# Kernel tuning notes

Measured on AMD Instinct MI355X. Metric: run time of the kernel, lower is better.

The kernel has to match this reference:

```python
import jax, jax.numpy as jnp
import numpy as np
import math

N_NODES = 100000
N_EDGES = 600000
HIDDEN = 128
HEADS = 8
HEAD_DIM = HIDDEN // HEADS
TEMPORAL = 32


def _xavier(key, fan_in, fan_out):
    bound = math.sqrt(6.0 / (fan_in + fan_out))
    return jax.random.uniform(key, (fan_in, fan_out), jnp.float32, -bound, bound)


def setup_inputs() -> dict:
    key = jax.random.key(0)
    ks = jax.random.split(key, 16)
    inp = {
        'query': jax.random.normal(ks[0], (N_NODES, HIDDEN), jnp.float32),
        'key': jax.random.normal(ks[1], (N_NODES, HIDDEN), jnp.float32),
        'value': jax.random.normal(ks[2], (N_NODES, HIDDEN), jnp.float32),
        'temporal_encoding': jax.random.normal(ks[3], (N_EDGES, TEMPORAL), jnp.float32),
        'edge_index': jax.random.randint(ks[4], (2, N_EDGES), 0, N_NODES, jnp.int64),
        # projection weights stored as [in, out] so y = x @ W + b
        'Wq': _xavier(ks[5], HIDDEN, HIDDEN), 'bq': jnp.zeros((HIDDEN,), jnp.float32),
        'Wk': _xavier(ks[6], HIDDEN, HIDDEN), 'bk': jnp.zeros((HIDDEN,), jnp.float32),
        'Wv': _xavier(ks[7], HIDDEN, HIDDEN), 'bv': jnp.zeros((HIDDEN,), jnp.float32),
        'Wtq': _xavier(ks[8], TEMPORAL, HIDDEN), 'btq': jnp.zeros((HIDDEN,), jnp.float32),
        'Wtk': _xavier(ks[9], TEMPORAL, HIDDEN), 'btk': jnp.zeros((HIDDEN,), jnp.float32),
        'Wout': _xavier(ks[10], HIDDEN, HIDDEN), 'bout': jnp.zeros((HIDDEN,), jnp.float32),
    }
    return inp


def reference(query, key, value, temporal_encoding, edge_index,
              Wq, bq, Wk, bk, Wv, bv, Wtq, btq, Wtk, btk, Wout, bout):
    n = query.shape[0]
    H, hd = HEADS, HEAD_DIM
    Q = (query @ Wq + bq).reshape(n, H, hd)
    K = (key @ Wk + bk).reshape(n, H, hd)
    V = (value @ Wv + bv).reshape(n, H, hd)
    tq = (temporal_encoding @ Wtq + btq).reshape(-1, H, hd)
    tk = (temporal_encoding @ Wtk + btk).reshape(-1, H, hd)

    src, tgt = edge_index[0], edge_index[1]
    # per-edge, per-head scores [E, H]
    scores = jnp.sum(Q[src] * K[tgt], axis=-1) / math.sqrt(hd)
    scores = scores + jnp.sum(tq * tk, axis=-1)

    # segment softmax over edges grouped by target node (stable, per head)
    seg_max = jax.ops.segment_max(scores, tgt, num_segments=n)  # [N, H]
    e = jnp.exp(scores - seg_max[tgt])
    seg_sum = jax.ops.segment_sum(e, tgt, num_segments=n)       # [N, H]
    attn_weights = e / seg_sum[tgt]                              # [E, H]

    # weighted scatter-add aggregation of source values onto targets
    agg = jax.ops.segment_sum(attn_weights[..., None] * V[src], tgt, num_segments=n)  # [N, H, hd]
    attn_output = agg.reshape(n, HIDDEN) @ Wout + bout
    return attn_output, attn_weights
```

## Files before the change

### kernel.cpp

```cpp
#include <hip/hip_runtime.h>
#include <hip/hip_bf16.h>

#define HID 128
#define MAXD 64

typedef __attribute__((ext_vector_type(8))) short bfrag8;
typedef __attribute__((ext_vector_type(4))) short bf4;
typedef __attribute__((ext_vector_type(4))) float facc4;

__device__ inline short f2bf(float x) {
  unsigned u = __builtin_bit_cast(unsigned, x);
  u += 0x7fffu + ((u >> 16) & 1u);
  return (short)(u >> 16);
}
__device__ inline float bf2f(short s) {
  unsigned u = ((unsigned)(unsigned short)s) << 16;
  return __builtin_bit_cast(float, u);
}

__device__ inline void store_val(float* Y, size_t i, float v) { Y[i] = v; }
__device__ inline void store_val(short* Y, size_t i, float v) { Y[i] = f2bf(v); }

__global__ __launch_bounds__(256) void init_k(
    const float* __restrict__ Wq, const float* __restrict__ Wk,
    const float* __restrict__ Wv, const float* __restrict__ Wout,
    const float* __restrict__ Wtq, const float* __restrict__ Wtk,
    short* __restrict__ out, int* __restrict__ degcur, int n2) {
  int gid = blockIdx.x * 256 + threadIdx.x;
  if (gid < n2) degcur[gid] = 0;
  if (gid >= 9216) return;
  bfrag8 v;
  if (gid < 8192) {
    int which = gid >> 11;
    int chunk = gid & 2047;
    const float* W = (which == 0) ? Wq : (which == 1) ? Wk
                   : (which == 2) ? Wv : Wout;
    int c  = chunk & 15;
    int g  = (chunk >> 4) & 3;
    int kt = (chunk >> 6) & 3;
    int ct = chunk >> 8;
    int col = ct * 16 + c;
    int k0 = kt * 32 + g * 8;
    #pragma unroll
    for (int i = 0; i < 8; ++i) v[i] = f2bf(W[(size_t)(k0 + i) * HID + col]);
  } else {
    int chunk = gid - 8192;
    int c  = chunk & 15;
    int g  = (chunk >> 4) & 3;
    int ct = (chunk >> 6) & 7;
    int qk = chunk >> 9;
    const float* W = qk ? Wtk : Wtq;
    int col = ct * 16 + c;
    int k0 = g * 8;
    #pragma unroll
    for (int i = 0; i < 8; ++i) v[i] = f2bf(W[(size_t)(k0 + i) * HID + col]);
  }
  *(bfrag8*)(out + (size_t)gid * 8) = v;
}

template <typename IT, typename OT, int MODE>
__device__ __forceinline__ void gemm_body(
    short* __restrict__ Ws, const IT* __restrict__ X,
    const short* __restrict__ Wp, const float* __restrict__ b,
    OT* __restrict__ Y, int nrows, int bx) {
  const int t = threadIdx.x;
  #pragma unroll
  for (int it = 0; it < 8; ++it) {
    int chunk = t + it * 256;
    *(bfrag8*)(&Ws[chunk * 8]) = *(const bfrag8*)(Wp + (size_t)chunk * 8);
  }
  __syncthreads();

  const int w  = t >> 6;
  const int l  = t & 63;
  const int lr = l & 15;
  const int g  = l >> 4;
  const int row0 = bx * 64 + w * 16;
  const int arow = min(row0 + lr, nrows - 1);

  facc4 acc[8];
  #pragma unroll
  for (int i = 0; i < 8; ++i) acc[i] = (facc4){0.f, 0.f, 0.f, 0.f};

  #pragma unroll
  for (int kt = 0; kt < 4; ++kt) {
    bfrag8 a;
    if constexpr (sizeof(IT) == 4) {
      const float* xp = (const float*)X + (size_t)arow * HID + kt * 32 + g * 8;
      float xv[8];
      *(facc4*)(xv)     = *(const facc4*)(xp);
      *(facc4*)(xv + 4) = *(const facc4*)(xp + 4);
      #pragma unroll
      for (int i = 0; i < 8; ++i) a[i] = f2bf(xv[i]);
    } else {
      a = *(const bfrag8*)((const short*)X + (size_t)arow * HID + kt * 32 + g * 8);
    }
    #pragma unroll
    for (int ct = 0; ct < 8; ++ct) {
      bfrag8 bf = *(const bfrag8*)(&Ws[(((ct * 4 + kt) * 4 + g) * 16 + lr) * 8]);
      acc[ct] = __builtin_amdgcn_mfma_f32_16x16x32_bf16(a, bf, acc[ct], 0, 0, 0);
    }
  }

  #pragma unroll
  for (int ct = 0; ct < 8; ++ct) {
    int col = ct * 16 + lr;
    float bias = b[col];
    #pragma unroll
    for (int r = 0; r < 4; ++r) {
      int row = row0 + g * 4 + r;
      if (row < nrows) {
        size_t oidx;
        if constexpr (MODE == 0) oidx = (size_t)row * HID + col;
        else oidx = (size_t)row * 256 + ((col >> 2) << 3) + (col & 3) +
                    (MODE == 2 ? 4 : 0);
        store_val(Y, oidx, acc[ct][r] + bias);
      }
    }
  }
}

__device__ __forceinline__ void temporal_body(
    short* __restrict__ Ws, float* __restrict__ bsh, float* __restrict__ tsh,
    const float* __restrict__ T, const short* __restrict__ Wp,
    const float* __restrict__ btq, const float* __restrict__ btk,
    float* __restrict__ ts, int E, int ntiles, int bx, int nblk) {
  const int t = threadIdx.x;
  #pragma unroll
  for (int it = 0; it < 4; ++it) {
    int chunk = t + it * 256;
    *(bfrag8*)(&Ws[chunk * 8]) = *(const bfrag8*)(Wp + (size_t)chunk * 8);
  }
  bsh[t] = (t < 128) ? btq[t] : btk[t - 128];
  __syncthreads();

  const int w = t >> 6;
  const int l = t & 63;
  const int c = l & 15;
  const int g = l >> 4;
  float* mytsh = tsh + w * 128;

  for (int tile = bx; tile < ntiles; tile += nblk) {
    const int e0 = tile * 64 + w * 16;
    const int ar = min(e0 + c, E - 1);
    const float* tp = T + (size_t)ar * 32 + g * 8;
    float xv[8];
    *(facc4*)(xv)     = *(const facc4*)(tp);
    *(facc4*)(xv + 4) = *(const facc4*)(tp + 4);
    bfrag8 tb;
    #pragma unroll
    for (int i = 0; i < 8; ++i) tb[i] = f2bf(xv[i]);

    #pragma unroll 1
    for (int ct = 0; ct < 8; ++ct) {
      facc4 accq = *(const facc4*)(&bsh[ct * 16 + g * 4]);
      bfrag8 wq = *(const bfrag8*)(&Ws[(ct * 64 + g * 16 + c) * 8]);
      accq = __builtin_amdgcn_mfma_f32_16x16x32_bf16(wq, tb, accq, 0, 0, 0);
      facc4 acck = *(const facc4*)(&bsh[128 + ct * 16 + g * 4]);
      bfrag8 wk = *(const bfrag8*)(&Ws[(512 + ct * 64 + g * 16 + c) * 8]);
      acck = __builtin_amdgcn_mfma_f32_16x16x32_bf16(wk, tb, acck, 0, 0, 0);

      float s = accq[0] * acck[0] + accq[1] * acck[1] +
                accq[2] * acck[2] + accq[3] * acck[3];
      s += __shfl_xor(s, 16, 64);
      s += __shfl_xor(s, 32, 64);
      if (g == 0) mytsh[c * 8 + ct] = s;
    }
    int e = e0 + (l >> 2);
    if (e < E) {
      float2 v2 = *(const float2*)(&mytsh[(l >> 2) * 8 + (l & 3) * 2]);
      *(float2*)(ts + (size_t)e0 * 8 + l * 2) = v2;
    }
  }
}

#define TBLK 2048
__global__ __launch_bounds__(256) void mega_k(
    const float* __restrict__ query, const float* __restrict__ key,
    const float* __restrict__ value, const float* __restrict__ temporal,
    const short* __restrict__ Wpre,
    const float* __restrict__ bq, const float* __restrict__ bk,
    const float* __restrict__ bv, const float* __restrict__ btq,
    const float* __restrict__ btk,
    short* __restrict__ QVp, short* __restrict__ Kp,
    float* __restrict__ tscores, const int* __restrict__ tgt,
    int* __restrict__ deg, int N, int E, int gblk, int ntiles) {
  __shared__ __align__(16) char smem[16384 * 2];
  const int bx = blockIdx.x;
  if (bx < gblk) {
    gemm_body<float, short, 1>((short*)smem, query, Wpre + 0 * 16384, bq, QVp, N, bx);
  } else if (bx < 2 * gblk) {
    gemm_body<float, short, 0>((short*)smem, key, Wpre + 1 * 16384, bk, Kp, N, bx - gblk);
  } else if (bx < 3 * gblk) {
    gemm_body<float, short, 2>((short*)smem, value, Wpre + 2 * 16384, bv, QVp, N, bx - 2 * gblk);
  } else if (bx < 3 * gblk + TBLK) {
    temporal_body((short*)smem, (float*)(smem + 16384), (float*)(smem + 16384 + 1024),
                  temporal, Wpre + 4 * 16384, btq, btk, tscores, E, ntiles,
                  bx - 3 * gblk, TBLK);
  } else {
    int gid = (bx - 3 * gblk - TBLK) * 256 + threadIdx.x;
    if (gid < E) atomicAdd(&deg[tgt[gid]], 1);
  }
}

template <typename IT, typename OT, int MODE>
__global__ __launch_bounds__(256) void gemm_mfma_k(
    const IT* __restrict__ X, const short* __restrict__ Wp,
    const float* __restrict__ b, OT* __restrict__ Y, int nrows) {
  __shared__ __align__(16) short Ws[16384];
  gemm_body<IT, OT, MODE>(Ws, X, Wp, b, Y, nrows, blockIdx.x);
}

__global__ __launch_bounds__(256) void block_sum_k(const int* __restrict__ deg,
                                                   int* __restrict__ bsum, int n) {
  __shared__ int sd[256];
  const int base = blockIdx.x * 1024;
  const int t = threadIdx.x;
  int s = 0;
  #pragma unroll
  for (int j = 0; j < 4; ++j) {
    int i = base + t + j * 256;
    if (i < n) s += deg[i];
  }
  sd[t] = s;
  __syncthreads();
  for (int st = 128; st; st >>= 1) {
    if (t < st) sd[t] += sd[t + st];
    __syncthreads();
  }
  if (t == 0) bsum[blockIdx.x] = sd[0];
}

__global__ __launch_bounds__(1024) void scan_partials_k(const int* __restrict__ bsum,
                                                        int* __restrict__ boff, int G) {
  __shared__ int sd[1024];
  const int t = threadIdx.x;
  int v = (t < G) ? bsum[t] : 0;
  sd[t] = v;
  __syncthreads();
  for (int s = 1; s < 1024; s <<= 1) {
    int a = (t >= s) ? sd[t - s] : 0;
    __syncthreads();
    sd[t] += a;
    __syncthreads();
  }
  if (t < G) boff[t] = sd[t] - v;
}

__global__ __launch_bounds__(256) void block_scan_k(const int* __restrict__ deg,
                                                    const int* __restrict__ boff,
                                                    int* __restrict__ off, int n) {
  __shared__ int sd[256];
  const int base = blockIdx.x * 1024;
  const int t = threadIdx.x;
  const int i0 = base + t * 4;
  int v[4];
  int s = 0;
  #pragma unroll
  for (int j = 0; j < 4; ++j) {
    v[j] = (i0 + j < n) ? deg[i0 + j] : 0;
    s += v[j];
  }
  const int own = s;
  sd[t] = s;
  __syncthreads();
  for (int st = 1; st < 256; st <<= 1) {
    int a = (t >= st) ? sd[t - st] : 0;
    __syncthreads();
    sd[t] += a;
    __syncthreads();
  }
  int acc = boff[blockIdx.x] + sd[t] - own;
  #pragma unroll
  for (int j = 0; j < 4; ++j) {
    int idx = i0 + j;
    if (idx < n) {
      off[idx] = acc;
      acc += v[j];
      if (idx == n - 1) off[n] = acc;
    }
  }
}

__global__ __launch_bounds__(256) void scatter_k(const int* __restrict__ src,
                                                 const int* __restrict__ tgt,
                                                 const int* __restrict__ off,
                                                 int* __restrict__ cur,
                                                 int2* __restrict__ elist2, int E) {
  int gid = blockIdx.x * 256 + threadIdx.x;
  if (gid < E) {
    int n = tgt[gid];
    int p = atomicAdd(&cur[n], 1);
    elist2[off[n] + p] = make_int2(gid, src[gid]);
  }
}

__global__ __launch_bounds__(256) void softmax_agg_k(
    const float* __restrict__ tscores, const short* __restrict__ QVp,
    const short* __restrict__ Kp, const int* __restrict__ off,
    const int2* __restrict__ elist2, float* __restrict__ attn_w,
    short* __restrict__ aggb, int N) {
  __shared__ int esh[8][MAXD];
  __shared__ int ssh[8][MAXD];
  __shared__ float sraw[8][MAXD][8];
  const int t = threadIdx.x;
  const int grp = t >> 5;
  const int g = t & 31;
  const int h = g >> 2;
  const int j = g & 3;
  const int n = blockIdx.x * 8 + grp;
  if (n >= N) return;

  const int s0 = off[n];
  const int deg = off[n + 1] - s0;

  float kr[4];
  {
    bf4 k4 = *(const bf4*)(Kp + (size_t)n * HID + g * 4);
    #pragma unroll
    for (int q = 0; q < 4; ++q) kr[q] = bf2f(k4[q]);
  }

  if (deg <= MAXD) {
    for (int i = g; i < deg; i += 32) {
      int2 es = elist2[s0 + i];
      esh[grp][i] = es.x;
      ssh[grp][i] = es.y;
    }

    float lsum = 0.f;
    float a0 = 0.f, a1 = 0.f, a2 = 0.f, a3 = 0.f;
    int i = 0;
    for (; i + 4 <= deg; i += 4) {
      bfrag8 qv0 = *(const bfrag8*)(QVp + (size_t)ssh[grp][i]     * 256 + g * 8);
      bfrag8 qv1 = *(const bfrag8*)(QVp + (size_t)ssh[grp][i + 1] * 256 + g * 8);
      bfrag8 qv2 = *(const bfrag8*)(QVp + (size_t)ssh[grp][i + 2] * 256 + g * 8);
      bfrag8 qv3 = *(const bfrag8*)(QVp + (size_t)ssh[grp][i + 3] * 256 + g * 8);
      float ts0 = tscores[(size_t)esh[grp][i]     * 8 + h];
      float ts1 = tscores[(size_t)esh[grp][i + 1] * 8 + h];
      float ts2 = tscores[(size_t)esh[grp][i + 2] * 8 + h];
      float ts3 = tscores[(size_t)esh[grp][i + 3] * 8 + h];
      float p0 = bf2f(qv0[0]) * kr[0] + bf2f(qv0[1]) * kr[1] +
                 bf2f(qv0[2]) * kr[2] + bf2f(qv0[3]) * kr[3];
      float p1 = bf2f(qv1[0]) * kr[0] + bf2f(qv1[1]) * kr[1] +
                 bf2f(qv1[2]) * kr[2] + bf2f(qv1[3]) * kr[3];
      float p2 = bf2f(qv2[0]) * kr[0] + bf2f(qv2[1]) * kr[1] +
                 bf2f(qv2[2]) * kr[2] + bf2f(qv2[3]) * kr[3];
      float p3 = bf2f(qv3[0]) * kr[0] + bf2f(qv3[1]) * kr[1] +
                 bf2f(qv3[2]) * kr[2] + bf2f(qv3[3]) * kr[3];
      p0 += __shfl_xor(p0, 1, 4); p0 += __shfl_xor(p0, 2, 4);
      p1 += __shfl_xor(p1, 1, 4); p1 += __shfl_xor(p1, 2, 4);
      p2 += __shfl_xor(p2, 1, 4); p2 += __shfl_xor(p2, 2, 4);
      p3 += __shfl_xor(p3, 1, 4); p3 += __shfl_xor(p3, 2, 4);
      float w0 = __expf(ts0 + p0 * 0.25f);
      float w1 = __expf(ts1 + p1 * 0.25f);
      float w2 = __expf(ts2 + p2 * 0.25f);
      float w3 = __expf(ts3 + p3 * 0.25f);
      if (j == 0) {
        sraw[grp][i][h]     = w0;
        sraw[grp][i + 1][h] = w1;
        sraw[grp][i + 2][h] = w2;
        sraw[grp][i + 3][h] = w3;
      }
      lsum += (w0 + w1) + (w2 + w3);
      a0 += w0 * bf2f(qv0[4]) + w1 * bf2f(qv1[4]) +
            w2 * bf2f(qv2[4]) + w3 * bf2f(qv3[4]);
      a1 += w0 * bf2f(qv0[5]) + w1 * bf2f(qv1[5]) +
            w2 * bf2f(qv2[5]) + w3 * bf2f(qv3[5]);
      a2 += w0 * bf2f(qv0[6]) + w1 * bf2f(qv1[6]) +
            w2 * bf2f(qv2[6]) + w3 * bf2f(qv3[6]);
      a3 += w0 * bf2f(qv0[7]) + w1 * bf2f(qv1[7]) +
            w2 * bf2f(qv2[7]) + w3 * bf2f(qv3[7]);
    }
    for (; i < deg; ++i) {
      bfrag8 qv0 = *(const bfrag8*)(QVp + (size_t)ssh[grp][i] * 256 + g * 8);
      float ts0 = tscores[(size_t)esh[grp][i] * 8 + h];
      float p0 = bf2f(qv0[0]) * kr[0] + bf2f(qv0[1]) * kr[1] +
                 bf2f(qv0[2]) * kr[2] + bf2f(qv0[3]) * kr[3];
      p0 += __shfl_xor(p0, 1, 4); p0 += __shfl_xor(p0, 2, 4);
      float w0 = __expf(ts0 + p0 * 0.25f);
      if (j == 0) sraw[grp][i][h] = w0;
      lsum += w0;
      a0 += w0 * bf2f(qv0[4]);
      a1 += w0 * bf2f(qv0[5]);
      a2 += w0 * bf2f(qv0[6]);
      a3 += w0 * bf2f(qv0[7]);
    }
    float invl = (lsum > 0.f) ? 1.0f / lsum : 0.f;

    bf4 st;
    st[0] = f2bf(a0 * invl); st[1] = f2bf(a1 * invl);
    st[2] = f2bf(a2 * invl); st[3] = f2bf(a3 * invl);
    *(bf4*)(aggb + (size_t)n * HID + g * 4) = st;

    if (j == 0) {
      for (int q = 0; q < deg; ++q)
        attn_w[(size_t)esh[grp][q] * 8 + h] = sraw[grp][q][h] * invl;
    }
  } else {
    float m = -3.0e38f;
    for (int q = 0; q < deg; ++q) {
      int2 es = elist2[s0 + q];
      bfrag8 q4 = *(const bfrag8*)(QVp + (size_t)es.y * 256 + g * 8);
      float p = bf2f(q4[0]) * kr[0] + bf2f(q4[1]) * kr[1] +
                bf2f(q4[2]) * kr[2] + bf2f(q4[3]) * kr[3];
      p += __shfl_xor(p, 1, 4); p += __shfl_xor(p, 2, 4);
      m = fmaxf(m, tscores[(size_t)es.x * 8 + h] + p * 0.25f);
    }
    float l = 0.f;
    for (int q = 0; q < deg; ++q) {
      int2 es = elist2[s0 + q];
      bfrag8 q4 = *(const bfrag8*)(QVp + (size_t)es.y * 256 + g * 8);
      float p = bf2f(q4[0]) * kr[0] + bf2f(q4[1]) * kr[1] +
                bf2f(q4[2]) * kr[2] + bf2f(q4[3]) * kr[3];
      p += __shfl_xor(p, 1, 4); p += __shfl_xor(p, 2, 4);
      l += __expf(tscores[(size_t)es.x * 8 + h] + p * 0.25f - m);
    }
    float invl = (l > 0.f) ? 1.0f / l : 0.f;
    float a0 = 0.f, a1 = 0.f, a2 = 0.f, a3 = 0.f;
    for (int q = 0; q < deg; ++q) {
      int2 es = elist2[s0 + q];
      bfrag8 q4 = *(const bfrag8*)(QVp + (size_t)es.y * 256 + g * 8);
      float p = bf2f(q4[0]) * kr[0] + bf2f(q4[1]) * kr[1] +
                bf2f(q4[2]) * kr[2] + bf2f(q4[3]) * kr[3];
      p += __shfl_xor(p, 1, 4); p += __shfl_xor(p, 2, 4);
      float w = __expf(tscores[(size_t)es.x * 8 + h] + p * 0.25f - m) * invl;
      a0 += w * bf2f(q4[4]);
      a1 += w * bf2f(q4[5]);
      a2 += w * bf2f(q4[6]);
      a3 += w * bf2f(q4[7]);
      if (j == 0) attn_w[(size_t)es.x * 8 + h] = w;
    }
    bf4 st;
    st[0] = f2bf(a0); st[1] = f2bf(a1); st[2] = f2bf(a2); st[3] = f2bf(a3);
    *(bf4*)(aggb + (size_t)n * HID + g * 4) = st;
  }
}

extern "C" void kernel_launch(void* const* d_in, const int* in_sizes, int n_in,
                              void* d_out, int out_size, void* d_ws, size_t ws_size,
                              hipStream_t stream) {
  const float* query    = (const float*)d_in[0];
  const float* key      = (const float*)d_in[1];
  const float* value    = (const float*)d_in[2];
  const float* temporal = (const float*)d_in[3];
  const int*   eidx     = (const int*)d_in[4];
  const float* Wq   = (const float*)d_in[5];
  const float* bq   = (const float*)d_in[6];
  const float* Wk   = (const float*)d_in[7];
  const float* bk   = (const float*)d_in[8];
  const float* Wv   = (const float*)d_in[9];
  const float* bv   = (const float*)d_in[10];
  const float* Wtq  = (const float*)d_in[11];
  const float* btq  = (const float*)d_in[12];
  const float* Wtk  = (const float*)d_in[13];
  const float* btk  = (const float*)d_in[14];
  const float* Wout = (const float*)d_in[15];
  const float* bout = (const float*)d_in[16];

  const int N = in_sizes[0] / HID;
  const int E = in_sizes[4] / 2;
  const int* src = eidx;
  const int* tgt = eidx + E;

  char* ws = (char*)d_ws;
  short* QVp = (short*)ws;                     ws += (size_t)N * 256 * 2;
  short* Kp = (short*)ws;                      ws += (size_t)N * HID * 2;
  short* aggb = (short*)ws;                    ws += (size_t)N * HID * 2;
  float* tscores = (float*)ws;                 ws += (size_t)E * 8 * 4;
  int* deg   = (int*)ws;                       ws += (size_t)N * 4;
  int* cur   = (int*)ws;                       ws += (size_t)N * 4;
  int* off   = (int*)ws;                       ws += (size_t)(N + 2) * 4;
  int2* elist2 = (int2*)ws;                    ws += (size_t)E * 8;
  int* bsum  = (int*)ws;                       ws += 1024 * 4;
  int* boff  = (int*)ws;                       ws += 1024 * 4;
  short* Wpre = (short*)ws;

  const int G = (N + 1023) / 1024;
  const int gblk = (N + 63) / 64;
  const int ntiles = (E + 63) / 64;
  const int cblk = (E + 255) / 256;

  dim3 b256(256);
  init_k<<<(2 * N + 255) / 256, b256, 0, stream>>>(Wq, Wk, Wv, Wout, Wtq, Wtk,
                                                   Wpre, deg, 2 * N);
  mega_k<<<3 * gblk + TBLK + cblk, b256, 0, stream>>>(
      query, key, value, temporal, Wpre, bq, bk, bv, btq, btk,
      QVp, Kp, tscores, tgt, deg, N, E, gblk, ntiles);

  block_sum_k<<<G, b256, 0, stream>>>(deg, bsum, N);
  scan_partials_k<<<1, 1024, 0, stream>>>(bsum, boff, G);
  block_scan_k<<<G, b256, 0, stream>>>(deg, boff, off, N);
  scatter_k<<<cblk, b256, 0, stream>>>(src, tgt, off, cur, elist2, E);

  float* attn_w = (float*)d_out + (size_t)N * HID;
  softmax_agg_k<<<(N + 7) / 8, b256, 0, stream>>>(tscores, QVp, Kp, off,
                                                  elist2, attn_w, aggb, N);

  gemm_mfma_k<short, float, 0><<<gblk, b256, 0, stream>>>(aggb, Wpre + 3 * 16384, bout,
                                                          (float*)d_out, N);
}
```

Before: 261.6 us.

## Persistent GEMM blocks, transposed MFMA output with vector stores, split QV layout

The projection GEMMs now loop over several 64-row chunks per block (a quarter as many blocks), so each block loads the packed weights into LDS once and reuses them. The MFMA operands are swapped so each lane holds four consecutive output columns of one row, which allows vectorized bias loads and 4-wide stores. The interleaved Q/V buffer becomes separate halves, [Q 128 | V 128] per node, and the aggregation kernels read Q and V as separate 8-byte loads. The temporal LDS scratch stride is padded from 8 to 10 to reduce bank conflicts. Fewer blocks may leave parts of the GPU idle and weaken latency hiding in the GEMMs.

```diff
diff --git a/kernel.cpp b/kernel.cpp
--- a/kernel.cpp
+++ b/kernel.cpp
@@ -3,6 +3,8 @@
 
 #define HID 128
 #define MAXD 64
+#define TBLK 2048
+#define CH 4
 
 typedef __attribute__((ext_vector_type(8))) short bfrag8;
 typedef __attribute__((ext_vector_type(4))) short bf4;
@@ -17,9 +19,6 @@
   unsigned u = ((unsigned)(unsigned short)s) << 16;
   return __builtin_bit_cast(float, u);
 }
-
-__device__ inline void store_val(float* Y, size_t i, float v) { Y[i] = v; }
-__device__ inline void store_val(short* Y, size_t i, float v) { Y[i] = f2bf(v); }
 
 __global__ __launch_bounds__(256) void init_k(
     const float* __restrict__ Wq, const float* __restrict__ Wk,
@@ -62,7 +61,7 @@
 __device__ __forceinline__ void gemm_body(
     short* __restrict__ Ws, const IT* __restrict__ X,
     const short* __restrict__ Wp, const float* __restrict__ b,
-    OT* __restrict__ Y, int nrows, int bx) {
+    OT* __restrict__ Y, int nrows, int bx0, int stride, int nchunks) {
   const int t = threadIdx.x;
   #pragma unroll
   for (int it = 0; it < 8; ++it) {
@@ -75,46 +74,55 @@
   const int l  = t & 63;
   const int lr = l & 15;
   const int g  = l >> 4;
-  const int row0 = bx * 64 + w * 16;
-  const int arow = min(row0 + lr, nrows - 1);
-
-  facc4 acc[8];
-  #pragma unroll
-  for (int i = 0; i < 8; ++i) acc[i] = (facc4){0.f, 0.f, 0.f, 0.f};
-
-  #pragma unroll
-  for (int kt = 0; kt < 4; ++kt) {
-    bfrag8 a;
-    if constexpr (sizeof(IT) == 4) {
-      const float* xp = (const float*)X + (size_t)arow * HID + kt * 32 + g * 8;
-      float xv[8];
-      *(facc4*)(xv)     = *(const facc4*)(xp);
-      *(facc4*)(xv + 4) = *(const facc4*)(xp + 4);
+
+  for (int ch = bx0; ch < nchunks; ch += stride) {
+    const int row0 = ch * 64 + w * 16;
+    const int arow = min(row0 + lr, nrows - 1);
+
+    facc4 acc[8];
+    #pragma unroll
+    for (int i = 0; i < 8; ++i) acc[i] = (facc4){0.f, 0.f, 0.f, 0.f};
+
+    #pragma unroll
+    for (int kt = 0; kt < 4; ++kt) {
+      bfrag8 a;
+      if constexpr (sizeof(IT) == 4) {
+        const float* xp = (const float*)X + (size_t)arow * HID + kt * 32 + g * 8;
+        float xv[8];
+        *(facc4*)(xv)     = *(const facc4*)(xp);
+        *(facc4*)(xv + 4) = *(const facc4*)(xp + 4);
+        #pragma unroll
+        for (int i = 0; i < 8; ++i) a[i] = f2bf(xv[i]);
+      } else {
+        a = *(const bfrag8*)((const short*)X + (size_t)arow * HID + kt * 32 + g * 8);
+      }
       #pragma unroll
-      for (int i = 0; i < 8; ++i) a[i] = f2bf(xv[i]);
-    } else {
-      a = *(const bfrag8*)((const short*)X + (size_t)arow * HID + kt * 32 + g * 8);
-    }
-    #pragma unroll
-    for (int ct = 0; ct < 8; ++ct) {
-      bfrag8 bf = *(const bfrag8*)(&Ws[(((ct * 4 + kt) * 4 + g) * 16 + lr) * 8]);
-      acc[ct] = __builtin_amdgcn_mfma_f32_16x16x32_bf16(a, bf, acc[ct], 0, 0, 0);
-    }
-  }
-
-  #pragma unroll
-  for (int ct = 0; ct < 8; ++ct) {
-    int col = ct * 16 + lr;
-    float bias = b[col];
-    #pragma unroll
-    for (int r = 0; r < 4; ++r) {
-      int row = row0 + g * 4 + r;
-      if (row < nrows) {
-        size_t oidx;
-        if constexpr (MODE == 0) oidx = (size_t)row * HID + col;
-        else oidx = (size_t)row * 256 + ((col >> 2) << 3) + (col & 3) +
-                    (MODE == 2 ? 4 : 0);
-        store_val(Y, oidx, acc[ct][r] + bias);
+      for (int ct = 0; ct < 8; ++ct) {
+        bfrag8 bf = *(const bfrag8*)(&Ws[(((ct * 4 + kt) * 4 + g) * 16 + lr) * 8]);
+        acc[ct] = __builtin_amdgcn_mfma_f32_16x16x32_bf16(bf, a, acc[ct], 0, 0, 0);
+      }
+    }
+
+    const int row = row0 + lr;
+    if (row < nrows) {
+      #pragma unroll
+      for (int ct = 0; ct < 8; ++ct) {
+        const int col0 = ct * 16 + g * 4;
+        facc4 bias = *(const facc4*)(b + col0);
+        facc4 v;
+        #pragma unroll
+        for (int j = 0; j < 4; ++j) v[j] = acc[ct][j] + bias[j];
+        if constexpr (sizeof(OT) == 4) {
+          *(facc4*)((float*)Y + (size_t)row * HID + col0) = v;
+        } else {
+          bf4 p;
+          #pragma unroll
+          for (int j = 0; j < 4; ++j) p[j] = f2bf(v[j]);
+          size_t base;
+          if constexpr (MODE == 0) base = (size_t)row * HID + col0;
+          else base = (size_t)row * 256 + col0 + (MODE == 2 ? 128 : 0);
+          *(bf4*)((short*)Y + base) = p;
+        }
       }
     }
   }
@@ -138,7 +146,7 @@
   const int l = t & 63;
   const int c = l & 15;
   const int g = l >> 4;
-  float* mytsh = tsh + w * 128;
+  float* mytsh = tsh + w * 160;
 
   for (int tile = bx; tile < ntiles; tile += nblk) {
     const int e0 = tile * 64 + w * 16;
@@ -164,17 +172,16 @@
                 accq[2] * acck[2] + accq[3] * acck[3];
       s += __shfl_xor(s, 16, 64);
       s += __shfl_xor(s, 32, 64);
-      if (g == 0) mytsh[c * 8 + ct] = s;
+      if (g == 0) mytsh[c * 10 + ct] = s;
     }
     int e = e0 + (l >> 2);
     if (e < E) {
-      float2 v2 = *(const float2*)(&mytsh[(l >> 2) * 8 + (l & 3) * 2]);
+      float2 v2 = *(const float2*)(&mytsh[(l >> 2) * 10 + (l & 3) * 2]);
       *(float2*)(ts + (size_t)e0 * 8 + l * 2) = v2;
     }
   }
 }
 
-#define TBLK 2048
 __global__ __launch_bounds__(256) void mega_k(
     const float* __restrict__ query, const float* __restrict__ key,
     const float* __restrict__ value, const float* __restrict__ temporal,
@@ -184,21 +191,25 @@
     const float* __restrict__ btk,
     short* __restrict__ QVp, short* __restrict__ Kp,
     float* __restrict__ tscores, const int* __restrict__ tgt,
-    int* __restrict__ deg, int N, int E, int gblk, int ntiles) {
-  __shared__ __align__(16) char smem[16384 * 2];
+    int* __restrict__ deg, int N, int E, int gq, int gblk, int ntiles) {
+  __shared__ __align__(16) char smem[32768];
   const int bx = blockIdx.x;
-  if (bx < gblk) {
-    gemm_body<float, short, 1>((short*)smem, query, Wpre + 0 * 16384, bq, QVp, N, bx);
-  } else if (bx < 2 * gblk) {
-    gemm_body<float, short, 0>((short*)smem, key, Wpre + 1 * 16384, bk, Kp, N, bx - gblk);
-  } else if (bx < 3 * gblk) {
-    gemm_body<float, short, 2>((short*)smem, value, Wpre + 2 * 16384, bv, QVp, N, bx - 2 * gblk);
-  } else if (bx < 3 * gblk + TBLK) {
-    temporal_body((short*)smem, (float*)(smem + 16384), (float*)(smem + 16384 + 1024),
+  if (bx < gq) {
+    gemm_body<float, short, 1>((short*)smem, query, Wpre + 0 * 16384, bq, QVp,
+                               N, bx, gq, gblk);
+  } else if (bx < 2 * gq) {
+    gemm_body<float, short, 0>((short*)smem, key, Wpre + 1 * 16384, bk, Kp,
+                               N, bx - gq, gq, gblk);
+  } else if (bx < 3 * gq) {
+    gemm_body<float, short, 2>((short*)smem, value, Wpre + 2 * 16384, bv, QVp,
+                               N, bx - 2 * gq, gq, gblk);
+  } else if (bx < 3 * gq + TBLK) {
+    temporal_body((short*)smem, (float*)(smem + 16384),
+                  (float*)(smem + 16384 + 1024),
                   temporal, Wpre + 4 * 16384, btq, btk, tscores, E, ntiles,
-                  bx - 3 * gblk, TBLK);
+                  bx - 3 * gq, TBLK);
   } else {
-    int gid = (bx - 3 * gblk - TBLK) * 256 + threadIdx.x;
+    int gid = (bx - 3 * gq - TBLK) * 256 + threadIdx.x;
     if (gid < E) atomicAdd(&deg[tgt[gid]], 1);
   }
 }
@@ -206,9 +217,10 @@
 template <typename IT, typename OT, int MODE>
 __global__ __launch_bounds__(256) void gemm_mfma_k(
     const IT* __restrict__ X, const short* __restrict__ Wp,
-    const float* __restrict__ b, OT* __restrict__ Y, int nrows) {
+    const float* __restrict__ b, OT* __restrict__ Y, int nrows,
+    int stride, int nchunks) {
   __shared__ __align__(16) short Ws[16384];
-  gemm_body<IT, OT, MODE>(Ws, X, Wp, b, Y, nrows, blockIdx.x);
+  gemm_body<IT, OT, MODE>(Ws, X, Wp, b, Y, nrows, blockIdx.x, stride, nchunks);
 }
 
 __global__ __launch_bounds__(256) void block_sum_k(const int* __restrict__ deg,
@@ -332,22 +344,30 @@
     float a0 = 0.f, a1 = 0.f, a2 = 0.f, a3 = 0.f;
     int i = 0;
     for (; i + 4 <= deg; i += 4) {
-      bfrag8 qv0 = *(const bfrag8*)(QVp + (size_t)ssh[grp][i]     * 256 + g * 8);
-      bfrag8 qv1 = *(const bfrag8*)(QVp + (size_t)ssh[grp][i + 1] * 256 + g * 8);
-      bfrag8 qv2 = *(const bfrag8*)(QVp + (size_t)ssh[grp][i + 2] * 256 + g * 8);
-      bfrag8 qv3 = *(const bfrag8*)(QVp + (size_t)ssh[grp][i + 3] * 256 + g * 8);
+      const size_t b0 = (size_t)ssh[grp][i]     * 256 + g * 4;
+      const size_t b1 = (size_t)ssh[grp][i + 1] * 256 + g * 4;
+      const size_t b2 = (size_t)ssh[grp][i + 2] * 256 + g * 4;
+      const size_t b3 = (size_t)ssh[grp][i + 3] * 256 + g * 4;
+      bf4 q0 = *(const bf4*)(QVp + b0);
+      bf4 q1 = *(const bf4*)(QVp + b1);
+      bf4 q2 = *(const bf4*)(QVp + b2);
+      bf4 q3 = *(const bf4*)(QVp + b3);
+      bf4 v0 = *(const bf4*)(QVp + b0 + 128);
+      bf4 v1 = *(const bf4*)(QVp + b1 + 128);
+      bf4 v2 = *(const bf4*)(QVp + b2 + 128);
+      bf4 v3 = *(const bf4*)(QVp + b3 + 128);
       float ts0 = tscores[(size_t)esh[grp][i]     * 8 + h];
       float ts1 = tscores[(size_t)esh[grp][i + 1] * 8 + h];
       float ts2 = tscores[(size_t)esh[grp][i + 2] * 8 + h];
       float ts3 = tscores[(size_t)esh[grp][i + 3] * 8 + h];
-      float p0 = bf2f(qv0[0]) * kr[0] + bf2f(qv0[1]) * kr[1] +
-                 bf2f(qv0[2]) * kr[2] + bf2f(qv0[3]) * kr[3];
-      float p1 = bf2f(qv1[0]) * kr[0] + bf2f(qv1[1]) * kr[1] +
-                 bf2f(qv1[2]) * kr[2] + bf2f(qv1[3]) * kr[3];
-      float p2 = bf2f(qv2[0]) * kr[0] + bf2f(qv2[1]) * kr[1] +
-                 bf2f(qv2[2]) * kr[2] + bf2f(qv2[3]) * kr[3];
-      float p3 = bf2f(qv3[0]) * kr[0] + bf2f(qv3[1]) * kr[1] +
-                 bf2f(qv3[2]) * kr[2] + bf2f(qv3[3]) * kr[3];
+      float p0 = bf2f(q0[0]) * kr[0] + bf2f(q0[1]) * kr[1] +
+                 bf2f(q0[2]) * kr[2] + bf2f(q0[3]) * kr[3];
+      float p1 = bf2f(q1[0]) * kr[0] + bf2f(q1[1]) * kr[1] +
+                 bf2f(q1[2]) * kr[2] + bf2f(q1[3]) * kr[3];
+      float p2 = bf2f(q2[0]) * kr[0] + bf2f(q2[1]) * kr[1] +
+                 bf2f(q2[2]) * kr[2] + bf2f(q2[3]) * kr[3];
+      float p3 = bf2f(q3[0]) * kr[0] + bf2f(q3[1]) * kr[1] +
+                 bf2f(q3[2]) * kr[2] + bf2f(q3[3]) * kr[3];
       p0 += __shfl_xor(p0, 1, 4); p0 += __shfl_xor(p0, 2, 4);
       p1 += __shfl_xor(p1, 1, 4); p1 += __shfl_xor(p1, 2, 4);
       p2 += __shfl_xor(p2, 1, 4); p2 += __shfl_xor(p2, 2, 4);
@@ -363,28 +383,30 @@
         sraw[grp][i + 3][h] = w3;
       }
       lsum += (w0 + w1) + (w2 + w3);
-      a0 += w0 * bf2f(qv0[4]) + w1 * bf2f(qv1[4]) +
-            w2 * bf2f(qv2[4]) + w3 * bf2f(qv3[4]);
-      a1 += w0 * bf2f(qv0[5]) + w1 * bf2f(qv1[5]) +
-            w2 * bf2f(qv2[5]) + w3 * bf2f(qv3[5]);
-      a2 += w0 * bf2f(qv0[6]) + w1 * bf2f(qv1[6]) +
-            w2 * bf2f(qv2[6]) + w3 * bf2f(qv3[6]);
-      a3 += w0 * bf2f(qv0[7]) + w1 * bf2f(qv1[7]) +
-            w2 * bf2f(qv2[7]) + w3 * bf2f(qv3[7]);
+      a0 += w0 * bf2f(v0[0]) + w1 * bf2f(v1[0]) +
+            w2 * bf2f(v2[0]) + w3 * bf2f(v3[0]);
+      a1 += w0 * bf2f(v0[1]) + w1 * bf2f(v1[1]) +
+            w2 * bf2f(v2[1]) + w3 * bf2f(v3[1]);
+      a2 += w0 * bf2f(v0[2]) + w1 * bf2f(v1[2]) +
+            w2 * bf2f(v2[2]) + w3 * bf2f(v3[2]);
+      a3 += w0 * bf2f(v0[3]) + w1 * bf2f(v1[3]) +
+            w2 * bf2f(v2[3]) + w3 * bf2f(v3[3]);
     }
     for (; i < deg; ++i) {
-      bfrag8 qv0 = *(const bfrag8*)(QVp + (size_t)ssh[grp][i] * 256 + g * 8);
+      const size_t b0 = (size_t)ssh[grp][i] * 256 + g * 4;
+      bf4 q0 = *(const bf4*)(QVp + b0);
+      bf4 v0 = *(const bf4*)(QVp + b0 + 128);
       float ts0 = tscores[(size_t)esh[grp][i] * 8 + h];
-      float p0 = bf2f(qv0[0]) * kr[0] + bf2f(qv0[1]) * kr[1] +
-                 bf2f(qv0[2]) * kr[2] + bf2f(qv0[3]) * kr[3];
+      float p0 = bf2f(q0[0]) * kr[0] + bf2f(q0[1]) * kr[1] +
+                 bf2f(q0[2]) * kr[2] + bf2f(q0[3]) * kr[3];
       p0 += __shfl_xor(p0, 1, 4); p0 += __shfl_xor(p0, 2, 4);
       float w0 = __expf(ts0 + p0 * 0.25f);
       if (j == 0) sraw[grp][i][h] = w0;
       lsum += w0;
-      a0 += w0 * bf2f(qv0[4]);
-      a1 += w0 * bf2f(qv0[5]);
-      a2 += w0 * bf2f(qv0[6]);
-      a3 += w0 * bf2f(qv0[7]);
+      a0 += w0 * bf2f(v0[0]);
+      a1 += w0 * bf2f(v0[1]);
+      a2 += w0 * bf2f(v0[2]);
+      a3 += w0 * bf2f(v0[3]);
     }
     float invl = (lsum > 0.f) ? 1.0f / lsum : 0.f;
 
@@ -401,7 +423,7 @@
     float m = -3.0e38f;
     for (int q = 0; q < deg; ++q) {
       int2 es = elist2[s0 + q];
-      bfrag8 q4 = *(const bfrag8*)(QVp + (size_t)es.y * 256 + g * 8);
+      bf4 q4 = *(const bf4*)(QVp + (size_t)es.y * 256 + g * 4);
       float p = bf2f(q4[0]) * kr[0] + bf2f(q4[1]) * kr[1] +
                 bf2f(q4[2]) * kr[2] + bf2f(q4[3]) * kr[3];
       p += __shfl_xor(p, 1, 4); p += __shfl_xor(p, 2, 4);
@@ -410,7 +432,7 @@
     float l = 0.f;
     for (int q = 0; q < deg; ++q) {
       int2 es = elist2[s0 + q];
-      bfrag8 q4 = *(const bfrag8*)(QVp + (size_t)es.y * 256 + g * 8);
+      bf4 q4 = *(const bf4*)(QVp + (size_t)es.y * 256 + g * 4);
       float p = bf2f(q4[0]) * kr[0] + bf2f(q4[1]) * kr[1] +
                 bf2f(q4[2]) * kr[2] + bf2f(q4[3]) * kr[3];
       p += __shfl_xor(p, 1, 4); p += __shfl_xor(p, 2, 4);
@@ -420,15 +442,16 @@
     float a0 = 0.f, a1 = 0.f, a2 = 0.f, a3 = 0.f;
     for (int q = 0; q < deg; ++q) {
       int2 es = elist2[s0 + q];
-      bfrag8 q4 = *(const bfrag8*)(QVp + (size_t)es.y * 256 + g * 8);
+      bf4 q4 = *(const bf4*)(QVp + (size_t)es.y * 256 + g * 4);
+      bf4 v4 = *(const bf4*)(QVp + (size_t)es.y * 256 + 128 + g * 4);
       float p = bf2f(q4[0]) * kr[0] + bf2f(q4[1]) * kr[1] +
                 bf2f(q4[2]) * kr[2] + bf2f(q4[3]) * kr[3];
       p += __shfl_xor(p, 1, 4); p += __shfl_xor(p, 2, 4);
       float w = __expf(tscores[(size_t)es.x * 8 + h] + p * 0.25f - m) * invl;
-      a0 += w * bf2f(q4[4]);
-      a1 += w * bf2f(q4[5]);
-      a2 += w * bf2f(q4[6]);
-      a3 += w * bf2f(q4[7]);
+      a0 += w * bf2f(v4[0]);
+      a1 += w * bf2f(v4[1]);
+      a2 += w * bf2f(v4[2]);
+      a3 += w * bf2f(v4[3]);
       if (j == 0) attn_w[(size_t)es.x * 8 + h] = w;
     }
     bf4 st;
@@ -478,15 +501,16 @@
 
   const int G = (N + 1023) / 1024;
   const int gblk = (N + 63) / 64;
+  const int gq = (gblk + CH - 1) / CH;
   const int ntiles = (E + 63) / 64;
   const int cblk = (E + 255) / 256;
 
   dim3 b256(256);
   init_k<<<(2 * N + 255) / 256, b256, 0, stream>>>(Wq, Wk, Wv, Wout, Wtq, Wtk,
                                                    Wpre, deg, 2 * N);
-  mega_k<<<3 * gblk + TBLK + cblk, b256, 0, stream>>>(
+  mega_k<<<3 * gq + TBLK + cblk, b256, 0, stream>>>(
       query, key, value, temporal, Wpre, bq, bk, bv, btq, btk,
-      QVp, Kp, tscores, tgt, deg, N, E, gblk, ntiles);
+      QVp, Kp, tscores, tgt, deg, N, E, gq, gblk, ntiles);
 
   block_sum_k<<<G, b256, 0, stream>>>(deg, bsum, N);
   scan_partials_k<<<1, 1024, 0, stream>>>(bsum, boff, G);
@@ -497,6 +521,7 @@
   softmax_agg_k<<<(N + 7) / 8, b256, 0, stream>>>(tscores, QVp, Kp, off,
                                                   elist2, attn_w, aggb, N);
 
-  gemm_mfma_k<short, float, 0><<<gblk, b256, 0, stream>>>(aggb, Wpre + 3 * 16384, bout,
-                                                          (float*)d_out, N);
-}
+  gemm_mfma_k<short, float, 0><<<gq, b256, 0, stream>>>(aggb, Wpre + 3 * 16384,
+                                                        bout, (float*)d_out, N,
+                                                        gq, gblk);
+}
```

Measured after the change: 254.1 us. 2.8% less time.
